# Performance work log

Measured on AMD Instinct MI355X. Metric: run time of the kernel, lower is better.

## Reference

```python
import jax, jax.numpy as jnp
import numpy as np

N, E = 50000, 800000
IN, H, C = 256, 8, 32  # heads=8, hidden_dim=32 -> out dim 256
NEG_SLOPE = 0.2
EPS = 1e-5


def setup_inputs() -> dict:
    key = jax.random.key(0)
    ks = jax.random.split(key, 6)
    x = jax.random.normal(ks[0], (N, IN), jnp.float32)
    edge_index = jax.random.randint(ks[1], (2, E), 0, N, dtype=jnp.int32)
    W = jax.random.normal(ks[2], (IN, H * C), jnp.float32) / np.sqrt(IN).astype(np.float32)
    att_src = jax.random.normal(ks[3], (H, C), jnp.float32) * 0.1
    att_dst = jax.random.normal(ks[4], (H, C), jnp.float32) * 0.1
    bias = jnp.zeros((H * C,), jnp.float32)
    gamma = jnp.ones((H * C,), jnp.float32)
    beta = jnp.zeros((H * C,), jnp.float32)
    return {"x": x, "edge_index": edge_index, "W": W, "att_src": att_src,
            "att_dst": att_dst, "bias": bias, "gamma": gamma, "beta": beta}


def reference(x, edge_index, W, att_src, att_dst, bias, gamma, beta):
    n = x.shape[0]
    # Linear projection -> per-head features [N, H, C]
    xl = (x @ W).reshape(n, H, C)
    # Per-node attention half-logits [N, H]
    a_src = jnp.einsum('nhc,hc->nh', xl, att_src)
    a_dst = jnp.einsum('nhc,hc->nh', xl, att_dst)
    # Add self loops (PyG GATConv default)
    loops = jnp.arange(n, dtype=edge_index.dtype)
    src = jnp.concatenate([edge_index[0], loops])  # [E+N]
    dst = jnp.concatenate([edge_index[1], loops])
    # Edge attention logits + segment softmax over destination neighborhoods
    logits = jax.nn.leaky_relu(a_src[src] + a_dst[dst], NEG_SLOPE)  # [E+N, H]
    seg_max = jax.ops.segment_max(logits, dst, num_segments=n)
    ex = jnp.exp(logits - seg_max[dst])
    denom = jax.ops.segment_sum(ex, dst, num_segments=n)
    alpha = ex / denom[dst]  # [E+N, H]
    # Weighted scatter-aggregation of source features
    msgs = xl[src] * alpha[:, :, None]  # [E+N, H, C]
    out = jax.ops.segment_sum(msgs, dst, num_segments=n).reshape(n, H * C) + bias
    # LayerNorm over feature dim
    mu = jnp.mean(out, axis=-1, keepdims=True)
    var = jnp.var(out, axis=-1, keepdims=True)
    return (out - mu) / jnp.sqrt(var + EPS) * gamma + beta
```

## Files before the change

### kernel.cpp

```cpp
#include <hip/hip_runtime.h>
#include <math.h>

#define NEG 0.2f
#define LNEPS 1e-5f
#define GB 512

typedef __attribute__((ext_vector_type(8))) short bf16x8;
typedef __attribute__((ext_vector_type(8))) unsigned short u16x8;
typedef __attribute__((ext_vector_type(4))) float f32x4;
typedef __attribute__((ext_vector_type(4))) unsigned int u32x4;

__device__ __forceinline__ float lrelu(float x){ return x > 0.f ? x : NEG*x; }

__device__ __forceinline__ short f2b(float f){
  unsigned u = __float_as_uint(f);
  unsigned r = u + 0x7fffu + ((u >> 16) & 1u);
  return (short)(r >> 16);
}
__device__ __forceinline__ float b2f(unsigned short u){
  return __uint_as_float(((unsigned)u) << 16);
}
__device__ __forceinline__ unsigned cvtpk(float lo, float hi){
  unsigned r;
  asm("v_cvt_pk_bf16_f32 %0, %1, %2" : "=v"(r) : "v"(lo), "v"(hi));
  return r;
}

__global__ __launch_bounds__(256) void wt_k(const float* __restrict__ W,
                                            const float* __restrict__ att_src,
                                            const float* __restrict__ att_dst,
                                            const int* __restrict__ dst,
                                            unsigned short* __restrict__ WTp,
                                            unsigned short* __restrict__ WSp,
                                            int* __restrict__ deg, int E){
  int b = blockIdx.x;
  int tid = threadIdx.x;
  if (b < 32){
    int g = b*256 + tid;
    int l = g & 63;
    int s = (g>>6) & 7;
    int j = (g>>9) & 3;
    int w = g >> 11;
    int col = w*64 + j*16 + (l & 15);
    int kb  = s*32 + (l>>4)*8;
    u16x8 v;
    #pragma unroll
    for (int e=0;e<8;e++) v[e] = (unsigned short)f2b(W[(size_t)(kb+e)*256 + col]);
    *(u16x8*)(WTp + (size_t)g*8) = v;
  } else if (b < 34){
    int g = (b-32)*256 + tid;
    int l = g & 63;
    int s = g >> 6;
    int col = l & 15;
    int kb  = s*32 + (l>>4)*8;
    int head = col & 7;
    const float* av = (col < 8 ? att_src : att_dst) + head*32;
    u16x8 v;
    #pragma unroll
    for (int e=0;e<8;e++){
      const float* wr = W + (size_t)(kb+e)*256 + head*32;
      float sum = 0.f;
      #pragma unroll
      for (int c2=0;c2<32;c2++) sum += wr[c2]*av[c2];
      v[e] = (unsigned short)f2b(sum);
    }
    *(u16x8*)(WSp + (size_t)g*8) = v;
  } else {
    int e = (b-34)*256 + tid;
    if (e < E) atomicAdd(&deg[dst[e]], 1);
  }
}

__global__ __launch_bounds__(1024) void scan1_k(const int* __restrict__ deg,
                                                int* __restrict__ off,
                                                int* __restrict__ bsum, int n){
  __shared__ int wsum[16];
  int tid=threadIdx.x, lane=tid&63, wid=tid>>6;
  int i = blockIdx.x*1024 + tid;
  int v = (i<n)?(deg[i]+1):0;
  int x = v;
  #pragma unroll
  for (int s=1;s<64;s<<=1){ int t2=__shfl_up(x,s); if (lane>=s) x+=t2; }
  if (lane==63) wsum[wid]=x;
  __syncthreads();
  if (tid<16){
    int y=wsum[tid];
    #pragma unroll
    for (int s=1;s<16;s<<=1){ int t2=__shfl_up(y,s); if (tid>=s) y+=t2; }
    wsum[tid]=y;
  }
  __syncthreads();
  int prefix=(wid? wsum[wid-1]:0);
  if (i<n) off[i]=prefix + x - v;
  if (tid==0) bsum[blockIdx.x]=wsum[15];
}

__global__ __launch_bounds__(1024) void scan3self_k(int* __restrict__ off,
    const int* __restrict__ bsum, int* __restrict__ sorted, int* __restrict__ cur,
    int n, int total){
  __shared__ int prefs;
  if (threadIdx.x < 64){
    int v = ((int)threadIdx.x < blockIdx.x) ? bsum[threadIdx.x] : 0;
    #pragma unroll
    for (int s=1;s<64;s<<=1) v += __shfl_xor(v, s);
    if (threadIdx.x==0) prefs = v;
  }
  __syncthreads();
  int i = blockIdx.x*1024 + threadIdx.x;
  if (blockIdx.x==0 && threadIdx.x==0) off[n] = total;
  if (i>=n) return;
  int o = off[i] + prefs;
  off[i] = o;
  sorted[o] = i;
  cur[i] = 1;
}

__device__ __forceinline__ void load_half(float4 nx[8], const float* p){
  #pragma unroll
  for (int s=0;s<4;s++){
    nx[2*s]   = *(const float4*)(p + s*32);
    nx[2*s+1] = *(const float4*)(p + s*32 + 4);
  }
}
__device__ __forceinline__ void cvt_half(bf16x8 af[4], const float4 nx[8]){
  #pragma unroll
  for (int s=0;s<4;s++){
    u32x4 q;
    q.x = cvtpk(nx[2*s].x,   nx[2*s].y);
    q.y = cvtpk(nx[2*s].z,   nx[2*s].w);
    q.z = cvtpk(nx[2*s+1].x, nx[2*s+1].y);
    q.w = cvtpk(nx[2*s+1].z, nx[2*s+1].w);
    af[s] = __builtin_bit_cast(bf16x8, q);
  }
}

__global__ __launch_bounds__(256, 2) void gemm_scat_k(const float* __restrict__ A,
    const unsigned short* __restrict__ WTp, const unsigned short* __restrict__ WSp,
    unsigned short* __restrict__ Cb,
    float* __restrict__ a_src, float* __restrict__ a_dst, int M, int nTiles,
    const int* __restrict__ src, const int* __restrict__ dst,
    const int* __restrict__ off, int* __restrict__ cur,
    int* __restrict__ sorted, int E){
  int tid = threadIdx.x;

  if (blockIdx.x >= GB){
    int e = (blockIdx.x - GB)*256 + tid;
    if (e < E){
      int d = dst[e];
      int pos = off[d] + atomicAdd(&cur[d], 1);
      sorted[pos] = src[e];
    }
    return;
  }

  int w   = tid >> 6;
  int l   = tid & 63;
  int l15 = l & 15;
  int kg  = l >> 4;
  int colbase = w*64;

  bf16x8 bfr[4][8];
  #pragma unroll
  for (int j=0;j<4;j++)
    #pragma unroll
    for (int ks=0;ks<8;ks++)
      bfr[j][ks] = *(const bf16x8*)(WTp + ((size_t)(((w*4+j)*8+ks)*64 + l))*8);

  bf16x8 bfa[8];
  if (w==0){
    #pragma unroll
    for (int ks=0;ks<8;ks++)
      bfa[ks] = *(const bf16x8*)(WSp + ((size_t)(ks*64 + l))*8);
  }

  int t = blockIdx.x;
  if (t >= nTiles) return;
  int row0 = t*16 + l15;
  const float* ap = A + (size_t)(row0 < M ? row0 : M-1)*256 + kg*8;
  float4 nx[8];
  load_half(nx, ap);

  while (t < nTiles){
    f32x4 acc[4];
    #pragma unroll
    for (int j=0;j<4;j++) acc[j] = (f32x4){0.f,0.f,0.f,0.f};
    f32x4 acc_a = (f32x4){0.f,0.f,0.f,0.f};
    bf16x8 af[4];

    cvt_half(af, nx);
    load_half(nx, ap + 128);
    #pragma unroll
    for (int s=0;s<4;s++){
      #pragma unroll
      for (int j=0;j<4;j++)
        acc[j] = __builtin_amdgcn_mfma_f32_16x16x32_bf16(bfr[j][s], af[s], acc[j], 0, 0, 0);
      if (w==0)
        acc_a = __builtin_amdgcn_mfma_f32_16x16x32_bf16(bfa[s], af[s], acc_a, 0, 0, 0);
    }

    int tn = t + GB;
    int rown = tn < nTiles ? tn*16 + l15 : row0;
    const float* apn = A + (size_t)(rown < M ? rown : M-1)*256 + kg*8;

    cvt_half(af, nx);
    load_half(nx, apn);
    #pragma unroll
    for (int s=0;s<4;s++){
      #pragma unroll
      for (int j=0;j<4;j++)
        acc[j] = __builtin_amdgcn_mfma_f32_16x16x32_bf16(bfr[j][4+s], af[s], acc[j], 0, 0, 0);
      if (w==0)
        acc_a = __builtin_amdgcn_mfma_f32_16x16x32_bf16(bfa[4+s], af[s], acc_a, 0, 0, 0);
    }

    int row = t*16 + l15;
    if (row < M){
      unsigned short* cp = Cb + (size_t)row*256 + colbase + kg*4;
      #pragma unroll
      for (int j=0;j<4;j++){
        uint2 pk;
        pk.x = cvtpk(acc[j][0], acc[j][1]);
        pk.y = cvtpk(acc[j][2], acc[j][3]);
        *(uint2*)(cp + j*16) = pk;
      }
      if (w==0){
        float4 av = {acc_a[0], acc_a[1], acc_a[2], acc_a[3]};
        float* dstp2 = (kg < 2 ? a_src : a_dst) + (size_t)row*8 + (kg&1)*4;
        *(float4*)dstp2 = av;
      }
    }
    t = tn; row0 = rown; ap = apn;
  }
}

__global__ __launch_bounds__(256) void agg5_k(const unsigned short* __restrict__ xlb,
    const float* __restrict__ a_src, const float* __restrict__ a_dst,
    const int* __restrict__ off, const int* __restrict__ sorted,
    const float* __restrict__ bias, const float* __restrict__ gamma,
    const float* __restrict__ beta, float* __restrict__ out, int n){
  int node = blockIdx.x*4 + (threadIdx.x>>6);
  if (node >= n) return;
  int lane = threadIdx.x & 63;
  int half = lane >> 5;
  int sl   = lane & 31;
  int h    = sl >> 2;
  int hh   = lane & 7;
  int je   = lane >> 3;
  float adst_h = a_dst[(size_t)node*8 + h];
  float adst_e = a_dst[(size_t)node*8 + hh];
  int s0 = off[node], dd = off[node+1] - s0;

  float acc[8] = {0.f,0.f,0.f,0.f,0.f,0.f,0.f,0.f};
  float den = 0.f;

  int i = 0;
  for (; i+8 <= dd; i += 8){
    int s[4];
    #pragma unroll
    for (int j=0;j<4;j++) s[j] = sorted[s0 + i + 2*j + half];
    int se = sorted[s0 + i + je];
    float w_l = __expf(lrelu(a_src[(size_t)se*8 + hh] + adst_e));
    float wv[4];
    #pragma unroll
    for (int j=0;j<4;j++) wv[j] = __shfl(w_l, ((2*j+half)<<3) | h);
    u16x8 u[4];
    #pragma unroll
    for (int j=0;j<4;j++) u[j] = *(const u16x8*)(xlb + (size_t)s[j]*256 + sl*8);
    #pragma unroll
    for (int j=0;j<4;j++){
      den += wv[j];
      #pragma unroll
      for (int k=0;k<8;k++) acc[k] += wv[j]*b2f((unsigned short)u[j][k]);
    }
  }
  for (; i < dd; i += 2){
    int idx = i + half;
    bool ok = idx < dd;
    int s1 = ok ? sorted[s0+idx] : node;
    float w1 = ok ? __expf(lrelu(a_src[(size_t)s1*8 + h] + adst_h)) : 0.f;
    u16x8 u1 = *(const u16x8*)(xlb + (size_t)s1*256 + sl*8);
    den += w1;
    #pragma unroll
    for (int k=0;k<8;k++) acc[k] += w1*b2f((unsigned short)u1[k]);
  }

  den += __shfl_xor(den, 32);
  #pragma unroll
  for (int k=0;k<8;k++) acc[k] += __shfl_xor(acc[k], 32);

  float rd = 1.0f/den;
  float4 bia0 = *(const float4*)(bias + sl*8);
  float4 bia1 = *(const float4*)(bias + sl*8 + 4);
  float o[8];
  o[0]=acc[0]*rd+bia0.x; o[1]=acc[1]*rd+bia0.y; o[2]=acc[2]*rd+bia0.z; o[3]=acc[3]*rd+bia0.w;
  o[4]=acc[4]*rd+bia1.x; o[5]=acc[5]*rd+bia1.y; o[6]=acc[6]*rd+bia1.z; o[7]=acc[7]*rd+bia1.w;

  float sum=0.f, ssq=0.f;
  #pragma unroll
  for (int k=0;k<8;k++){ sum += o[k]; ssq += o[k]*o[k]; }
  #pragma unroll
  for (int s=1;s<32;s<<=1){ sum += __shfl_xor(sum,s); ssq += __shfl_xor(ssq,s); }
  float mean = sum*(1.0f/256.0f);
  float var  = ssq*(1.0f/256.0f) - mean*mean;
  float rstd = rsqrtf(var + LNEPS);

  int f = sl*8 + half*4;
  float4 g  = *(const float4*)(gamma + f);
  float4 be = *(const float4*)(beta + f);
  int kb = half*4;
  float4 ov;
  ov.x = (o[kb+0]-mean)*rstd*g.x+be.x;
  ov.y = (o[kb+1]-mean)*rstd*g.y+be.y;
  ov.z = (o[kb+2]-mean)*rstd*g.z+be.z;
  ov.w = (o[kb+3]-mean)*rstd*g.w+be.w;
  *(float4*)(out + (size_t)node*256 + f) = ov;
}

extern "C" void kernel_launch(void* const* d_in, const int* in_sizes, int n_in,
                              void* d_out, int out_size, void* d_ws, size_t ws_size,
                              hipStream_t stream){
  const float* x       = (const float*)d_in[0];
  const int*   ei      = (const int*)  d_in[1];
  const float* W       = (const float*)d_in[2];
  const float* att_src = (const float*)d_in[3];
  const float* att_dst = (const float*)d_in[4];
  const float* bias    = (const float*)d_in[5];
  const float* gamma   = (const float*)d_in[6];
  const float* beta    = (const float*)d_in[7];
  float* out = (float*)d_out;

  int N = in_sizes[0]/256;
  int E = in_sizes[1]/2;
  const int* srcp = ei;
  const int* dstp = ei + E;

  unsigned short* xlb = (unsigned short*)d_ws;
  float* a_src = (float*)(xlb + (size_t)N*256);
  float* a_dst = a_src + (size_t)N*8;
  int*   deg   = (int*)(a_dst + (size_t)N*8);
  int*   off   = deg + N;
  int*   cur   = off + N + 1;
  int*   sorted= cur + N;
  int*   bsum  = sorted + E + N;
  unsigned short* WTp = (unsigned short*)(bsum + 1024);
  unsigned short* WSp = WTp + 65536;

  int nb = (N + 1023)/1024;
  int nTiles = (N + 15)/16;
  int scatBlocks = (E + 255)/256;

  hipMemsetAsync(deg, 0, (size_t)N*sizeof(int), stream);
  wt_k<<<34 + scatBlocks, 256, 0, stream>>>(W, att_src, att_dst, dstp, WTp, WSp, deg, E);
  scan1_k<<<nb, 1024, 0, stream>>>(deg, off, bsum, N);
  scan3self_k<<<nb, 1024, 0, stream>>>(off, bsum, sorted, cur, N, E + N);
  gemm_scat_k<<<GB + scatBlocks, 256, 0, stream>>>(x, WTp, WSp, xlb, a_src, a_dst,
                                                   N, nTiles, srcp, dstp, off, cur,
                                                   sorted, E);
  agg5_k<<<(N+3)/4, 256, 0, stream>>>(xlb, a_src, a_dst, off, sorted, bias, gamma, beta, out, N);
}
```

Before: 188.5 us.

## Split fused GEMM/scatter kernel into separate scatter and one-tile-per-block GEMM

Separates the edge scatter from the projection GEMM into its own kernel launch. The GEMM becomes one 16-row tile per block across all tiles instead of a persistent grid of 512 blocks, and it loads weight fragments on demand instead of preloading them into registers. This removes the persistent loop and the large register footprint, but adds a kernel launch, drops the overlap between scatter and GEMM, and reloads W fragments from cache in every block.

```diff
diff --git a/kernel.cpp b/kernel.cpp
--- a/kernel.cpp
+++ b/kernel.cpp
@@ -3,7 +3,6 @@
 
 #define NEG 0.2f
 #define LNEPS 1e-5f
-#define GB 512
 
 typedef __attribute__((ext_vector_type(8))) short bf16x8;
 typedef __attribute__((ext_vector_type(8))) unsigned short u16x8;
@@ -115,6 +114,17 @@
   cur[i] = 1;
 }
 
+__global__ void scat_k(const int* __restrict__ src, const int* __restrict__ dst,
+                       const int* __restrict__ off, int* __restrict__ cur,
+                       int* __restrict__ sorted, int E){
+  int e = blockIdx.x*256 + threadIdx.x;
+  if (e < E){
+    int d = dst[e];
+    int pos = off[d] + atomicAdd(&cur[d], 1);
+    sorted[pos] = src[e];
+  }
+}
+
 __device__ __forceinline__ void load_half(float4 nx[8], const float* p){
   #pragma unroll
   for (int s=0;s<4;s++){
@@ -134,102 +144,73 @@
   }
 }
 
-__global__ __launch_bounds__(256, 2) void gemm_scat_k(const float* __restrict__ A,
+__global__ __launch_bounds__(256, 2) void gemm_k(const float* __restrict__ A,
     const unsigned short* __restrict__ WTp, const unsigned short* __restrict__ WSp,
     unsigned short* __restrict__ Cb,
-    float* __restrict__ a_src, float* __restrict__ a_dst, int M, int nTiles,
-    const int* __restrict__ src, const int* __restrict__ dst,
-    const int* __restrict__ off, int* __restrict__ cur,
-    int* __restrict__ sorted, int E){
+    float* __restrict__ a_src, float* __restrict__ a_dst, int M){
   int tid = threadIdx.x;
-
-  if (blockIdx.x >= GB){
-    int e = (blockIdx.x - GB)*256 + tid;
-    if (e < E){
-      int d = dst[e];
-      int pos = off[d] + atomicAdd(&cur[d], 1);
-      sorted[pos] = src[e];
-    }
-    return;
-  }
-
   int w   = tid >> 6;
   int l   = tid & 63;
   int l15 = l & 15;
   int kg  = l >> 4;
   int colbase = w*64;
-
-  bf16x8 bfr[4][8];
-  #pragma unroll
-  for (int j=0;j<4;j++)
-    #pragma unroll
-    for (int ks=0;ks<8;ks++)
-      bfr[j][ks] = *(const bf16x8*)(WTp + ((size_t)(((w*4+j)*8+ks)*64 + l))*8);
-
-  bf16x8 bfa[8];
-  if (w==0){
-    #pragma unroll
-    for (int ks=0;ks<8;ks++)
-      bfa[ks] = *(const bf16x8*)(WSp + ((size_t)(ks*64 + l))*8);
-  }
-
   int t = blockIdx.x;
-  if (t >= nTiles) return;
-  int row0 = t*16 + l15;
-  const float* ap = A + (size_t)(row0 < M ? row0 : M-1)*256 + kg*8;
-  float4 nx[8];
+
+  int row = t*16 + l15;
+  int arow = row < M ? row : M-1;
+  const float* ap = A + (size_t)arow*256 + kg*8;
+
+  float4 nx[8], ny[8];
   load_half(nx, ap);
-
-  while (t < nTiles){
-    f32x4 acc[4];
-    #pragma unroll
-    for (int j=0;j<4;j++) acc[j] = (f32x4){0.f,0.f,0.f,0.f};
-    f32x4 acc_a = (f32x4){0.f,0.f,0.f,0.f};
-    bf16x8 af[4];
-
-    cvt_half(af, nx);
-    load_half(nx, ap + 128);
-    #pragma unroll
-    for (int s=0;s<4;s++){
-      #pragma unroll
-      for (int j=0;j<4;j++)
-        acc[j] = __builtin_amdgcn_mfma_f32_16x16x32_bf16(bfr[j][s], af[s], acc[j], 0, 0, 0);
-      if (w==0)
-        acc_a = __builtin_amdgcn_mfma_f32_16x16x32_bf16(bfa[s], af[s], acc_a, 0, 0, 0);
-    }
-
-    int tn = t + GB;
-    int rown = tn < nTiles ? tn*16 + l15 : row0;
-    const float* apn = A + (size_t)(rown < M ? rown : M-1)*256 + kg*8;
-
-    cvt_half(af, nx);
-    load_half(nx, apn);
-    #pragma unroll
-    for (int s=0;s<4;s++){
-      #pragma unroll
-      for (int j=0;j<4;j++)
-        acc[j] = __builtin_amdgcn_mfma_f32_16x16x32_bf16(bfr[j][4+s], af[s], acc[j], 0, 0, 0);
-      if (w==0)
-        acc_a = __builtin_amdgcn_mfma_f32_16x16x32_bf16(bfa[4+s], af[s], acc_a, 0, 0, 0);
-    }
-
-    int row = t*16 + l15;
-    if (row < M){
-      unsigned short* cp = Cb + (size_t)row*256 + colbase + kg*4;
-      #pragma unroll
-      for (int j=0;j<4;j++){
-        uint2 pk;
-        pk.x = cvtpk(acc[j][0], acc[j][1]);
-        pk.y = cvtpk(acc[j][2], acc[j][3]);
-        *(uint2*)(cp + j*16) = pk;
-      }
-      if (w==0){
-        float4 av = {acc_a[0], acc_a[1], acc_a[2], acc_a[3]};
-        float* dstp2 = (kg < 2 ? a_src : a_dst) + (size_t)row*8 + (kg&1)*4;
-        *(float4*)dstp2 = av;
-      }
-    }
-    t = tn; row0 = rown; ap = apn;
+  load_half(ny, ap + 128);
+
+  f32x4 acc[4];
+  #pragma unroll
+  for (int j=0;j<4;j++) acc[j] = (f32x4){0.f,0.f,0.f,0.f};
+  f32x4 acc_a = (f32x4){0.f,0.f,0.f,0.f};
+  bf16x8 af[4];
+
+  cvt_half(af, nx);
+  #pragma unroll
+  for (int s=0;s<4;s++){
+    #pragma unroll
+    for (int j=0;j<4;j++){
+      bf16x8 bf = *(const bf16x8*)(WTp + ((size_t)(((w*4+j)*8+s)*64 + l))*8);
+      acc[j] = __builtin_amdgcn_mfma_f32_16x16x32_bf16(bf, af[s], acc[j], 0, 0, 0);
+    }
+    if (w==0){
+      bf16x8 ba = *(const bf16x8*)(WSp + ((size_t)(s*64 + l))*8);
+      acc_a = __builtin_amdgcn_mfma_f32_16x16x32_bf16(ba, af[s], acc_a, 0, 0, 0);
+    }
+  }
+  cvt_half(af, ny);
+  #pragma unroll
+  for (int s=0;s<4;s++){
+    #pragma unroll
+    for (int j=0;j<4;j++){
+      bf16x8 bf = *(const bf16x8*)(WTp + ((size_t)(((w*4+j)*8+4+s)*64 + l))*8);
+      acc[j] = __builtin_amdgcn_mfma_f32_16x16x32_bf16(bf, af[s], acc[j], 0, 0, 0);
+    }
+    if (w==0){
+      bf16x8 ba = *(const bf16x8*)(WSp + ((size_t)((4+s)*64 + l))*8);
+      acc_a = __builtin_amdgcn_mfma_f32_16x16x32_bf16(ba, af[s], acc_a, 0, 0, 0);
+    }
+  }
+
+  if (row < M){
+    unsigned short* cp = Cb + (size_t)row*256 + colbase + kg*4;
+    #pragma unroll
+    for (int j=0;j<4;j++){
+      uint2 pk;
+      pk.x = cvtpk(acc[j][0], acc[j][1]);
+      pk.y = cvtpk(acc[j][2], acc[j][3]);
+      *(uint2*)(cp + j*16) = pk;
+    }
+    if (w==0){
+      float4 av = {acc_a[0], acc_a[1], acc_a[2], acc_a[3]};
+      float* dstp2 = (kg < 2 ? a_src : a_dst) + (size_t)row*8 + (kg&1)*4;
+      *(float4*)dstp2 = av;
+    }
   }
 }
 
@@ -353,8 +334,7 @@
   wt_k<<<34 + scatBlocks, 256, 0, stream>>>(W, att_src, att_dst, dstp, WTp, WSp, deg, E);
   scan1_k<<<nb, 1024, 0, stream>>>(deg, off, bsum, N);
   scan3self_k<<<nb, 1024, 0, stream>>>(off, bsum, sorted, cur, N, E + N);
-  gemm_scat_k<<<GB + scatBlocks, 256, 0, stream>>>(x, WTp, WSp, xlb, a_src, a_dst,
-                                                   N, nTiles, srcp, dstp, off, cur,
-                                                   sorted, E);
+  scat_k<<<scatBlocks, 256, 0, stream>>>(srcp, dstp, off, cur, sorted, E);
+  gemm_k<<<nTiles, 256, 0, stream>>>(x, WTp, WSp, xlb, a_src, a_dst, N);
   agg5_k<<<(N+3)/4, 256, 0, stream>>>(xlb, a_src, a_dst, off, sorted, bias, gamma, beta, out, N);
 }
```

Measured after the change: 210.2 us. 1.12x slower.
